# Optimization experiments

Measured on AMD Instinct MI355X. Metric: run time of the kernel, lower is better.

The kernel has to match this reference:

```python
import jax, jax.numpy as jnp
import numpy as np

EPS = 1e-8  # torch F.cosine_similarity eps


def setup_inputs() -> dict:
    key = jax.random.key(0)
    B, CAP, CD, CTX = 32, 32768, 64, 64
    ks = jax.random.split(key, 9)
    inp = {
        "query_content": jax.random.normal(ks[0], (B, CD), jnp.float32),
        "query_context": jax.random.normal(ks[1], (B, CTX), jnp.float32),
        "memory_content": 0.1 * jax.random.normal(ks[2], (CAP, CD), jnp.float32),
        "memory_contexts": 0.1 * jax.random.normal(ks[3], (CAP, CTX), jnp.float32),
        "memory_freshness": jnp.ones((CAP,), jnp.float32),
        "W1": jax.random.normal(ks[4], (2 * CD, CD), jnp.float32) / np.sqrt(2 * CD),
        "b1": 0.01 * jax.random.normal(ks[5], (CD,), jnp.float32),
        "W2": jax.random.normal(ks[6], (CD, 1), jnp.float32) / np.sqrt(CD),
        "b2": 0.01 * jax.random.normal(ks[7], (1,), jnp.float32),
        "top_k": 16,
    }
    return inp


def reference(query_content, query_context, memory_content, memory_contexts,
              memory_freshness, W1, b1, W2, b2, top_k):
    B, CD = query_content.shape
    # similarity_calculator MLP over all (query, memory) pairs.
    # Linear on concat([q, m]) == q @ W1[:CD] + m @ W1[CD:]  (avoids the concat).
    q_part = query_content @ W1[:CD]            # [B, CD]
    m_part = memory_content @ W1[CD:]           # [CAP, CD]
    h = jax.nn.relu(q_part[:, None, :] + m_part[None, :, :] + b1)  # [B, CAP, CD]
    content_sim = jax.nn.sigmoid(jnp.einsum('bch,h->bc', h, W2[:, 0]) + b2[0])  # [B, CAP]

    # cosine similarity between query_context and each stored context
    qn = query_context / jnp.maximum(jnp.linalg.norm(query_context, axis=-1, keepdims=True), EPS)
    mn = memory_contexts / jnp.maximum(jnp.linalg.norm(memory_contexts, axis=-1, keepdims=True), EPS)
    context_sim = qn @ mn.T                      # [B, CAP]

    time_weights = memory_freshness              # time_mask is all-ones in source
    final = 0.5 * content_sim + 0.3 * context_sim + 0.2 * time_weights[None, :]

    top_similarities, top_indices = jax.lax.top_k(final, top_k)   # [B, k]
    retrieved_content = memory_content[top_indices]               # [B, k, CD]
    retrieved_time_weights = time_weights[top_indices]            # [B, k]
    return (retrieved_content, top_similarities, retrieved_time_weights)
```

## Files before the change

kernel.cpp:

```cpp
#include <hip/hip_runtime.h>
#include <math.h>

#define CAP   32768
#define NB    32
#define ROWS  64
#define NBLK  (CAP / ROWS)
#define TOPK  16
#define CEPS  1e-8f

#define PITCH 68
#define CHUNK 2048
#define NCHUNK (CAP / CHUNK)

#define WS_QP    0
#define WS_QN    2048
#define WS_FINAL 4096

__global__ __launch_bounds__(64) void prep_kernel(
    const float* __restrict__ qc,
    const float* __restrict__ qctx,
    const float* __restrict__ W1,
    const float* __restrict__ b1,
    float* __restrict__ ws)
{
    const int b = blockIdx.x;
    const int j = threadIdx.x;

    float a0 = b1[j], a1 = 0.f, a2 = 0.f, a3 = 0.f;
    #pragma unroll
    for (int i = 0; i < 64; i += 4) {
        a0 = fmaf(qc[b * 64 + i + 0], W1[(i + 0) * 64 + j], a0);
        a1 = fmaf(qc[b * 64 + i + 1], W1[(i + 1) * 64 + j], a1);
        a2 = fmaf(qc[b * 64 + i + 2], W1[(i + 2) * 64 + j], a2);
        a3 = fmaf(qc[b * 64 + i + 3], W1[(i + 3) * 64 + j], a3);
    }
    ws[WS_QP + b * 64 + j] = (a0 + a1) + (a2 + a3);

    float x = qctx[b * 64 + j];
    float ss = x * x;
    ss += __shfl_xor(ss, 1,  64);
    ss += __shfl_xor(ss, 2,  64);
    ss += __shfl_xor(ss, 4,  64);
    ss += __shfl_xor(ss, 8,  64);
    ss += __shfl_xor(ss, 16, 64);
    ss += __shfl_xor(ss, 32, 64);
    ws[WS_QN + b * 64 + j] = x / fmaxf(sqrtf(ss), CEPS);
}

__global__ __launch_bounds__(256) void score_kernel(
    const float* __restrict__ mcont,
    const float* __restrict__ mctx,
    const float* __restrict__ fresh,
    const float* __restrict__ W1,
    const float* __restrict__ W2,
    const float* __restrict__ b2,
    float* __restrict__ ws)
{
    __shared__ float s_mc[ROWS * PITCH];
    __shared__ float s_qp[NB * PITCH];
    __shared__ float s_qn[NB * PITCH];
    __shared__ float s_base[ROWS];
    __shared__ float s_inv[ROWS];

    const int tid = threadIdx.x;
    const int C0 = blockIdx.x * ROWS;

    const float4* g_mc = (const float4*)(mcont + (size_t)C0 * 64);
    #pragma unroll
    for (int t = tid; t < ROWS * 16; t += 256) {
        int r = t >> 4, c4 = t & 15;
        *(float4*)&s_mc[r * PITCH + c4 * 4] = g_mc[t];
    }
    const float4* g_qp = (const float4*)(ws + WS_QP);
    const float4* g_qn = (const float4*)(ws + WS_QN);
    #pragma unroll
    for (int t = tid; t < NB * 16; t += 256) {
        int r = t >> 4, c4 = t & 15;
        *(float4*)&s_qp[r * PITCH + c4 * 4] = g_qp[t];
        *(float4*)&s_qn[r * PITCH + c4 * 4] = g_qn[t];
    }
    {
        const int r = tid >> 2, q = tid & 3;
        const float* xr = mctx + (size_t)(C0 + r) * 64 + q * 16;
        float ss = 0.f;
        #pragma unroll
        for (int i = 0; i < 4; ++i) {
            float4 x = *(const float4*)&xr[i * 4];
            ss = fmaf(x.x, x.x, ss); ss = fmaf(x.y, x.y, ss);
            ss = fmaf(x.z, x.z, ss); ss = fmaf(x.w, x.w, ss);
        }
        ss += __shfl_xor(ss, 1, 64);
        ss += __shfl_xor(ss, 2, 64);
        if (q == 0) {
            s_inv[r]  = 0.3f / fmaxf(sqrtf(ss), CEPS);
            s_base[r] = 0.2f * fresh[C0 + r];
        }
    }
    __syncthreads();

    const int c_lo = tid & 15;
    const int j0 = (tid >> 4) * 4;
    {
        float acc[4][4] = {{0.f}};
        #pragma unroll 4
        for (int i4 = 0; i4 < 16; ++i4) {
            float4 w0 = *(const float4*)&W1[(64 + i4 * 4 + 0) * 64 + j0];
            float4 w1r = *(const float4*)&W1[(64 + i4 * 4 + 1) * 64 + j0];
            float4 w2r = *(const float4*)&W1[(64 + i4 * 4 + 2) * 64 + j0];
            float4 w3r = *(const float4*)&W1[(64 + i4 * 4 + 3) * 64 + j0];
            #pragma unroll
            for (int ci = 0; ci < 4; ++ci) {
                float4 m = *(const float4*)&s_mc[(c_lo + 16 * ci) * PITCH + i4 * 4];
                acc[ci][0] = fmaf(m.x, w0.x, acc[ci][0]);
                acc[ci][1] = fmaf(m.x, w0.y, acc[ci][1]);
                acc[ci][2] = fmaf(m.x, w0.z, acc[ci][2]);
                acc[ci][3] = fmaf(m.x, w0.w, acc[ci][3]);
                acc[ci][0] = fmaf(m.y, w1r.x, acc[ci][0]);
                acc[ci][1] = fmaf(m.y, w1r.y, acc[ci][1]);
                acc[ci][2] = fmaf(m.y, w1r.z, acc[ci][2]);
                acc[ci][3] = fmaf(m.y, w1r.w, acc[ci][3]);
                acc[ci][0] = fmaf(m.z, w2r.x, acc[ci][0]);
                acc[ci][1] = fmaf(m.z, w2r.y, acc[ci][1]);
                acc[ci][2] = fmaf(m.z, w2r.z, acc[ci][2]);
                acc[ci][3] = fmaf(m.z, w2r.w, acc[ci][3]);
                acc[ci][0] = fmaf(m.w, w3r.x, acc[ci][0]);
                acc[ci][1] = fmaf(m.w, w3r.y, acc[ci][1]);
                acc[ci][2] = fmaf(m.w, w3r.z, acc[ci][2]);
                acc[ci][3] = fmaf(m.w, w3r.w, acc[ci][3]);
            }
        }
        __syncthreads();
        #pragma unroll
        for (int jj = 0; jj < 4; ++jj)
            #pragma unroll
            for (int ci = 0; ci < 4; ++ci)
                s_mc[(j0 + jj) * PITCH + c_lo + 16 * ci] = acc[ci][jj];
    }
    __syncthreads();

    const int bq = (tid & 15) << 1;
    const int cq = (tid >> 4) << 2;
    float4 a1v[2];
    a1v[0] = make_float4(0.f, 0.f, 0.f, 0.f);
    a1v[1] = make_float4(0.f, 0.f, 0.f, 0.f);
    float a2[2][4] = {{0.f}};
    const float* mxb = mctx + (size_t)C0 * 64;

    #pragma unroll 4
    for (int j4 = 0; j4 < 16; ++j4) {
        const int jo = j4 * 4;
        float4 w2v = *(const float4*)(W2 + jo);
        float4 qp0 = *(const float4*)&s_qp[ bq      * PITCH + jo];
        float4 qp1 = *(const float4*)&s_qp[(bq + 1) * PITCH + jo];
        float4 qn0 = *(const float4*)&s_qn[ bq      * PITCH + jo];
        float4 qn1 = *(const float4*)&s_qn[(bq + 1) * PITCH + jo];
        float4 m0 = *(const float4*)&s_mc[(jo + 0) * PITCH + cq];
        float4 m1 = *(const float4*)&s_mc[(jo + 1) * PITCH + cq];
        float4 m2 = *(const float4*)&s_mc[(jo + 2) * PITCH + cq];
        float4 m3 = *(const float4*)&s_mc[(jo + 3) * PITCH + cq];

        #pragma unroll
        for (int bi = 0; bi < 2; ++bi) {
            float4 qp = bi ? qp1 : qp0;
            float4& av = a1v[bi];
            av.x = fmaf(fmaxf(qp.x + m0.x, 0.f), w2v.x, av.x);
            av.y = fmaf(fmaxf(qp.x + m0.y, 0.f), w2v.x, av.y);
            av.z = fmaf(fmaxf(qp.x + m0.z, 0.f), w2v.x, av.z);
            av.w = fmaf(fmaxf(qp.x + m0.w, 0.f), w2v.x, av.w);
            av.x = fmaf(fmaxf(qp.y + m1.x, 0.f), w2v.y, av.x);
            av.y = fmaf(fmaxf(qp.y + m1.y, 0.f), w2v.y, av.y);
            av.z = fmaf(fmaxf(qp.y + m1.z, 0.f), w2v.y, av.z);
            av.w = fmaf(fmaxf(qp.y + m1.w, 0.f), w2v.y, av.w);
            av.x = fmaf(fmaxf(qp.z + m2.x, 0.f), w2v.z, av.x);
            av.y = fmaf(fmaxf(qp.z + m2.y, 0.f), w2v.z, av.y);
            av.z = fmaf(fmaxf(qp.z + m2.z, 0.f), w2v.z, av.z);
            av.w = fmaf(fmaxf(qp.z + m2.w, 0.f), w2v.z, av.w);
            av.x = fmaf(fmaxf(qp.w + m3.x, 0.f), w2v.w, av.x);
            av.y = fmaf(fmaxf(qp.w + m3.y, 0.f), w2v.w, av.y);
            av.z = fmaf(fmaxf(qp.w + m3.z, 0.f), w2v.w, av.z);
            av.w = fmaf(fmaxf(qp.w + m3.w, 0.f), w2v.w, av.w);
        }
        #pragma unroll
        for (int ci = 0; ci < 4; ++ci) {
            float4 xv = *(const float4*)&mxb[(cq + ci) * 64 + jo];
            a2[0][ci] = fmaf(qn0.x, xv.x, a2[0][ci]);
            a2[0][ci] = fmaf(qn0.y, xv.y, a2[0][ci]);
            a2[0][ci] = fmaf(qn0.z, xv.z, a2[0][ci]);
            a2[0][ci] = fmaf(qn0.w, xv.w, a2[0][ci]);
            a2[1][ci] = fmaf(qn1.x, xv.x, a2[1][ci]);
            a2[1][ci] = fmaf(qn1.y, xv.y, a2[1][ci]);
            a2[1][ci] = fmaf(qn1.z, xv.z, a2[1][ci]);
            a2[1][ci] = fmaf(qn1.w, xv.w, a2[1][ci]);
        }
    }

    const float b2v = b2[0];
    float4 inv4  = *(const float4*)&s_inv[cq];
    float4 base4 = *(const float4*)&s_base[cq];
    #pragma unroll
    for (int bi = 0; bi < 2; ++bi) {
        float4 r;
        r.x = 0.5f / (1.f + expf(-(a1v[bi].x + b2v))) + a2[bi][0] * inv4.x + base4.x;
        r.y = 0.5f / (1.f + expf(-(a1v[bi].y + b2v))) + a2[bi][1] * inv4.y + base4.y;
        r.z = 0.5f / (1.f + expf(-(a1v[bi].z + b2v))) + a2[bi][2] * inv4.z + base4.z;
        r.w = 0.5f / (1.f + expf(-(a1v[bi].w + b2v))) + a2[bi][3] * inv4.w + base4.w;
        *(float4*)&ws[WS_FINAL + (size_t)(bq + bi) * CAP + C0 + cq] = r;
    }
}

__global__ __launch_bounds__(64) void topk_part1(float* __restrict__ ws)
{
    const int lane = threadIdx.x;
    const int b = blockIdx.y;
    float* row = ws + WS_FINAL + (size_t)b * CAP;
    const int cbase = blockIdx.x * CHUNK;

    float v[32];
    #pragma unroll
    for (int g = 0; g < 8; ++g) {
        float4 t = *(const float4*)&row[cbase + g * 256 + lane * 4];
        v[4 * g + 0] = t.x; v[4 * g + 1] = t.y;
        v[4 * g + 2] = t.z; v[4 * g + 3] = t.w;
    }

    float outv = 0.f;
    int   outi = 0;

    for (int k = 0; k < TOPK; ++k) {
        float bv = v[0]; int bj = 0;
        #pragma unroll
        for (int j = 1; j < 32; ++j)
            if (v[j] > bv) { bv = v[j]; bj = j; }
        int bi = cbase + (bj >> 2) * 256 + lane * 4 + (bj & 3);

        #pragma unroll
        for (int off = 1; off < 64; off <<= 1) {
            float ov = __shfl_xor(bv, off, 64);
            int   oi = __shfl_xor(bi, off, 64);
            if (ov > bv || (ov == bv && oi < bi)) { bv = ov; bi = oi; }
        }
        if (lane == k) { outv = bv; outi = bi; }

        int rel = bi - cbase;
        bool mine = (((rel >> 2) & 63) == lane);
        int wj = ((rel >> 8) << 2) | (rel & 3);
        #pragma unroll
        for (int j = 0; j < 32; ++j)
            if (mine && wj == j) v[j] = -INFINITY;
    }

    if (lane < TOPK) {
        row[cbase + lane]        = outv;
        row[cbase + TOPK + lane] = __int_as_float(outi);
    }
}

__global__ __launch_bounds__(64) void topk_part2(
    const float* __restrict__ mcont,
    const float* __restrict__ fresh,
    const float* __restrict__ ws,
    float* __restrict__ out)
{
    const int lane = threadIdx.x;
    const int b = blockIdx.x;
    const float* row = ws + WS_FINAL + (size_t)b * CAP;

    float* out_content = out;
    float* out_sim     = out + NB * TOPK * 64;
    float* out_tw      = out + NB * TOPK * 64 + NB * TOPK;

    const int chunk = lane & 15;
    const int s0 = lane >> 4;
    float v[4]; int iv[4];
    #pragma unroll
    for (int s = 0; s < 4; ++s) {
        v[s]  = row[chunk * CHUNK + s0 + 4 * s];
        iv[s] = __float_as_int(row[chunk * CHUNK + TOPK + s0 + 4 * s]);
    }

    float wval = 0.f; int widx = 0;
    for (int k = 0; k < TOPK; ++k) {
        float bv = v[0]; int bi = iv[0];
        #pragma unroll
        for (int s = 1; s < 4; ++s)
            if (v[s] > bv || (v[s] == bv && iv[s] < bi)) { bv = v[s]; bi = iv[s]; }
        #pragma unroll
        for (int off = 1; off < 64; off <<= 1) {
            float ov = __shfl_xor(bv, off, 64);
            int   oi = __shfl_xor(bi, off, 64);
            if (ov > bv || (ov == bv && oi < bi)) { bv = ov; bi = oi; }
        }
        if (lane == k) { wval = bv; widx = bi; }
        #pragma unroll
        for (int s = 0; s < 4; ++s)
            if (iv[s] == bi) v[s] = -INFINITY;
    }

    if (lane < TOPK) {
        out_sim[b * TOPK + lane] = wval;
        out_tw [b * TOPK + lane] = fresh[widx];
    }

    #pragma unroll
    for (int r = 0; r < TOPK; ++r) {
        int wi = __shfl(widx, r, 64);
        out_content[(size_t)b * TOPK * 64 + r * 64 + lane] =
            mcont[(size_t)wi * 64 + lane];
    }
}

extern "C" void kernel_launch(void* const* d_in, const int* in_sizes, int n_in,
                              void* d_out, int out_size, void* d_ws, size_t ws_size,
                              hipStream_t stream) {
    const float* qc    = (const float*)d_in[0];
    const float* qctx  = (const float*)d_in[1];
    const float* mcont = (const float*)d_in[2];
    const float* mctx  = (const float*)d_in[3];
    const float* fresh = (const float*)d_in[4];
    const float* W1    = (const float*)d_in[5];
    const float* b1    = (const float*)d_in[6];
    const float* W2    = (const float*)d_in[7];
    const float* b2    = (const float*)d_in[8];
    float* out = (float*)d_out;
    float* ws  = (float*)d_ws;

    prep_kernel<<<NB, 64, 0, stream>>>(qc, qctx, W1, b1, ws);
    score_kernel<<<NBLK, 256, 0, stream>>>(mcont, mctx, fresh, W1, W2, b2, ws);
    topk_part1<<<dim3(NCHUNK, NB), 64, 0, stream>>>(ws);
    topk_part2<<<NB, 64, 0, stream>>>(mcont, fresh, ws, out);
}
```

Baseline: 138.1 us.

## Fuse query prep into score kernel and halve top-k chunk size

Removes the separate prep kernel launch: every score block now recomputes the query projection q@W1[:64]+b1 and the normalized query context directly into shared memory, with each wave caching a W1 column in registers. The top-k first stage switches to 1024-element chunks, which doubles the number of partial blocks and halves the per-lane work, while the second stage merges 512 candidates over 8 slots per lane. This trades a kernel launch and a global round trip for redundant per-block compute (512 blocks × 32×64×64 FMAs) and extra register pressure under launch_bounds(256,2).

New measurement: 143.0 us. +3.6%, slower.

```diff
diff --git a/kernel.cpp b/kernel.cpp
--- a/kernel.cpp
+++ b/kernel.cpp
@@ -9,49 +9,19 @@
 #define CEPS  1e-8f
 
 #define PITCH 68
-#define CHUNK 2048
+#define CHUNK 1024
 #define NCHUNK (CAP / CHUNK)
 
-#define WS_QP    0
-#define WS_QN    2048
-#define WS_FINAL 4096
-
-__global__ __launch_bounds__(64) void prep_kernel(
+#define WS_FINAL 0
+
+__global__ __launch_bounds__(256, 2) void score_kernel(
     const float* __restrict__ qc,
     const float* __restrict__ qctx,
-    const float* __restrict__ W1,
-    const float* __restrict__ b1,
-    float* __restrict__ ws)
-{
-    const int b = blockIdx.x;
-    const int j = threadIdx.x;
-
-    float a0 = b1[j], a1 = 0.f, a2 = 0.f, a3 = 0.f;
-    #pragma unroll
-    for (int i = 0; i < 64; i += 4) {
-        a0 = fmaf(qc[b * 64 + i + 0], W1[(i + 0) * 64 + j], a0);
-        a1 = fmaf(qc[b * 64 + i + 1], W1[(i + 1) * 64 + j], a1);
-        a2 = fmaf(qc[b * 64 + i + 2], W1[(i + 2) * 64 + j], a2);
-        a3 = fmaf(qc[b * 64 + i + 3], W1[(i + 3) * 64 + j], a3);
-    }
-    ws[WS_QP + b * 64 + j] = (a0 + a1) + (a2 + a3);
-
-    float x = qctx[b * 64 + j];
-    float ss = x * x;
-    ss += __shfl_xor(ss, 1,  64);
-    ss += __shfl_xor(ss, 2,  64);
-    ss += __shfl_xor(ss, 4,  64);
-    ss += __shfl_xor(ss, 8,  64);
-    ss += __shfl_xor(ss, 16, 64);
-    ss += __shfl_xor(ss, 32, 64);
-    ws[WS_QN + b * 64 + j] = x / fmaxf(sqrtf(ss), CEPS);
-}
-
-__global__ __launch_bounds__(256) void score_kernel(
     const float* __restrict__ mcont,
     const float* __restrict__ mctx,
     const float* __restrict__ fresh,
     const float* __restrict__ W1,
+    const float* __restrict__ b1,
     const float* __restrict__ W2,
     const float* __restrict__ b2,
     float* __restrict__ ws)
@@ -71,14 +41,6 @@
         int r = t >> 4, c4 = t & 15;
         *(float4*)&s_mc[r * PITCH + c4 * 4] = g_mc[t];
     }
-    const float4* g_qp = (const float4*)(ws + WS_QP);
-    const float4* g_qn = (const float4*)(ws + WS_QN);
-    #pragma unroll
-    for (int t = tid; t < NB * 16; t += 256) {
-        int r = t >> 4, c4 = t & 15;
-        *(float4*)&s_qp[r * PITCH + c4 * 4] = g_qp[t];
-        *(float4*)&s_qn[r * PITCH + c4 * 4] = g_qn[t];
-    }
     {
         const int r = tid >> 2, q = tid & 3;
         const float* xr = mctx + (size_t)(C0 + r) * 64 + q * 16;
@@ -94,6 +56,40 @@
         if (q == 0) {
             s_inv[r]  = 0.3f / fmaxf(sqrtf(ss), CEPS);
             s_base[r] = 0.2f * fresh[C0 + r];
+        }
+    }
+
+    {
+        const int lane = tid & 63;
+        const int wv = tid >> 6;
+        float w1c[64];
+        #pragma unroll
+        for (int i = 0; i < 64; ++i) w1c[i] = W1[i * 64 + lane];
+        const float b1v = b1[lane];
+        #pragma unroll
+        for (int bb = 0; bb < 8; ++bb) {
+            const int b = wv * 8 + bb;
+            const float4* qc4 = (const float4*)(qc + b * 64);
+            float a0 = b1v, a1 = 0.f, a2 = 0.f, a3 = 0.f;
+            #pragma unroll
+            for (int i4 = 0; i4 < 16; ++i4) {
+                float4 q4 = qc4[i4];
+                a0 = fmaf(q4.x, w1c[4 * i4 + 0], a0);
+                a1 = fmaf(q4.y, w1c[4 * i4 + 1], a1);
+                a2 = fmaf(q4.z, w1c[4 * i4 + 2], a2);
+                a3 = fmaf(q4.w, w1c[4 * i4 + 3], a3);
+            }
+            s_qp[b * PITCH + lane] = (a0 + a1) + (a2 + a3);
+
+            float x = qctx[b * 64 + lane];
+            float ss = x * x;
+            ss += __shfl_xor(ss, 1,  64);
+            ss += __shfl_xor(ss, 2,  64);
+            ss += __shfl_xor(ss, 4,  64);
+            ss += __shfl_xor(ss, 8,  64);
+            ss += __shfl_xor(ss, 16, 64);
+            ss += __shfl_xor(ss, 32, 64);
+            s_qn[b * PITCH + lane] = x / fmaxf(sqrtf(ss), CEPS);
         }
     }
     __syncthreads();
@@ -215,9 +211,9 @@
     float* row = ws + WS_FINAL + (size_t)b * CAP;
     const int cbase = blockIdx.x * CHUNK;
 
-    float v[32];
-    #pragma unroll
-    for (int g = 0; g < 8; ++g) {
+    float v[16];
+    #pragma unroll
+    for (int g = 0; g < 4; ++g) {
         float4 t = *(const float4*)&row[cbase + g * 256 + lane * 4];
         v[4 * g + 0] = t.x; v[4 * g + 1] = t.y;
         v[4 * g + 2] = t.z; v[4 * g + 3] = t.w;
@@ -229,7 +225,7 @@
     for (int k = 0; k < TOPK; ++k) {
         float bv = v[0]; int bj = 0;
         #pragma unroll
-        for (int j = 1; j < 32; ++j)
+        for (int j = 1; j < 16; ++j)
             if (v[j] > bv) { bv = v[j]; bj = j; }
         int bi = cbase + (bj >> 2) * 256 + lane * 4 + (bj & 3);
 
@@ -245,7 +241,7 @@
         bool mine = (((rel >> 2) & 63) == lane);
         int wj = ((rel >> 8) << 2) | (rel & 3);
         #pragma unroll
-        for (int j = 0; j < 32; ++j)
+        for (int j = 0; j < 16; ++j)
             if (mine && wj == j) v[j] = -INFINITY;
     }
 
@@ -269,20 +265,20 @@
     float* out_sim     = out + NB * TOPK * 64;
     float* out_tw      = out + NB * TOPK * 64 + NB * TOPK;
 
-    const int chunk = lane & 15;
-    const int s0 = lane >> 4;
-    float v[4]; int iv[4];
-    #pragma unroll
-    for (int s = 0; s < 4; ++s) {
-        v[s]  = row[chunk * CHUNK + s0 + 4 * s];
-        iv[s] = __float_as_int(row[chunk * CHUNK + TOPK + s0 + 4 * s]);
+    float v[8]; int iv[8];
+    #pragma unroll
+    for (int s = 0; s < 8; ++s) {
+        int cand = s * 64 + lane;
+        int ch = cand >> 4, pos = cand & 15;
+        v[s]  = row[ch * CHUNK + pos];
+        iv[s] = __float_as_int(row[ch * CHUNK + TOPK + pos]);
     }
 
     float wval = 0.f; int widx = 0;
     for (int k = 0; k < TOPK; ++k) {
         float bv = v[0]; int bi = iv[0];
         #pragma unroll
-        for (int s = 1; s < 4; ++s)
+        for (int s = 1; s < 8; ++s)
             if (v[s] > bv || (v[s] == bv && iv[s] < bi)) { bv = v[s]; bi = iv[s]; }
         #pragma unroll
         for (int off = 1; off < 64; off <<= 1) {
@@ -292,7 +288,7 @@
         }
         if (lane == k) { wval = bv; widx = bi; }
         #pragma unroll
-        for (int s = 0; s < 4; ++s)
+        for (int s = 0; s < 8; ++s)
             if (iv[s] == bi) v[s] = -INFINITY;
     }
 
@@ -324,8 +320,8 @@
     float* out = (float*)d_out;
     float* ws  = (float*)d_ws;
 
-    prep_kernel<<<NB, 64, 0, stream>>>(qc, qctx, W1, b1, ws);
-    score_kernel<<<NBLK, 256, 0, stream>>>(mcont, mctx, fresh, W1, W2, b2, ws);
+    score_kernel<<<NBLK, 256, 0, stream>>>(qc, qctx, mcont, mctx, fresh,
+                                           W1, b1, W2, b2, ws);
     topk_part1<<<dim3(NCHUNK, NB), 64, 0, stream>>>(ws);
     topk_part2<<<NB, 64, 0, stream>>>(mcont, fresh, ws, out);
 }
```
